# Kernel optimization log

Measured on AMD Instinct MI355X. Metric: run time of the kernel, lower is better.

## Reference

```python
import jax, jax.numpy as jnp
import numpy as np

B, N, P, Q, E = 8, 5000, 256, 256, 160000


def _linear_params(k, out_d, in_d):
    # matches nn.init.normal_(std=0.1) weights, zero bias
    return 0.1 * jax.random.normal(k, (out_d, in_d), jnp.float32), jnp.zeros((out_d,), jnp.float32)


def setup_inputs() -> dict:
    key = jax.random.key(0)
    ks = jax.random.split(key, 8)
    u = jax.random.normal(ks[0], (B, N, P + Q), jnp.float32)
    src = jax.random.randint(ks[1], (E,), 0, N, dtype=jnp.int32)
    dst = jax.random.randint(ks[2], (E,), 0, N, dtype=jnp.int32)
    t = jnp.zeros((1,), jnp.float32)
    W_Fc, b_Fc = _linear_params(ks[3], P, P + Q)
    W_Fh, b_Fh = _linear_params(ks[4], Q, P + Q)
    W_Gc, b_Gc = _linear_params(ks[5], P, P + Q)
    W_Z, b_Z = _linear_params(ks[6], P, P + Q)
    W_A, b_A = _linear_params(ks[7], Q, 2 * Q)
    return dict(u=u, src=src, dst=dst, t=t,
                W_Fc=W_Fc, b_Fc=b_Fc, W_Fh=W_Fh, b_Fh=b_Fh,
                W_Gc=W_Gc, b_Gc=b_Gc, W_Z=W_Z, b_Z=b_Z,
                W_A=W_A, b_A=b_A)


def _neighbor_mean(h, src, dst):
    # h: [B, N, Q] -> mean over in-neighbors per node (zeros if no neighbors)
    hT = jnp.transpose(h, (1, 0, 2))            # [N, B, Q]
    msgs = hT[src]                              # [E, B, Q] gather
    summed = jax.ops.segment_sum(msgs, dst, num_segments=N)          # [N, B, Q]
    deg = jax.ops.segment_sum(jnp.ones((E,), h.dtype), dst, num_segments=N)  # [N]
    mean = summed / jnp.maximum(deg, 1.0)[:, None, None]
    return jnp.transpose(mean, (1, 0, 2))       # [B, N, Q]


def reference(u, src, dst, t, W_Fc, b_Fc, W_Fh, b_Fh, W_Gc, b_Gc, W_Z, b_Z, W_A, b_A):
    sp = jax.nn.softplus
    lin = lambda x, W, b: jnp.einsum('bnd,od->bno', x, W) + b
    c = u[:, :, :P]
    h = u[:, :, P:]
    agg = _neighbor_mean(h, src, dst)                           # [B, N, Q]
    h_ = sp(lin(jnp.concatenate([h, agg], axis=2), W_A, b_A))   # [B, N, Q]
    u_ = jnp.concatenate([c, h_], axis=2)                       # [B, N, P+Q]
    Fc = sp(lin(u_, W_Fc, b_Fc))
    Gc = sp(lin(u_, W_Gc, b_Gc))
    Zt = jnp.tanh(lin(u_, W_Z, b_Z))
    Fh = sp(lin(u_, W_Fh, b_Fh))
    dc = -Fc * c + Gc * Zt
    dh = -Fh * h
    # tangent projection: remove component of dc along c
    proj = jnp.sum(dc * c, axis=2, keepdims=True) / jnp.sum(c * c, axis=2, keepdims=True)
    dc = dc - proj * c
    return jnp.concatenate([dc, dh], axis=2)
```

## Files before the change

kernel.cpp:

```cpp
#include <hip/hip_runtime.h>
#include <math.h>

#define B_ 8
#define N_ 5000
#define E_ 160000
#define M_ 40000
#define K_ 512
#define XT_ 313

typedef __bf16 v8bf __attribute__((ext_vector_type(8)));
typedef float  v4f  __attribute__((ext_vector_type(4)));
typedef unsigned short u16x4v __attribute__((ext_vector_type(4)));
typedef unsigned short u16x8v __attribute__((ext_vector_type(8)));

__device__ __forceinline__ unsigned short f2b(float f){
  unsigned int u = __builtin_bit_cast(unsigned int, f);
  u += 0x7FFFu + ((u >> 16) & 1u);
  return (unsigned short)(u >> 16);
}
__device__ __forceinline__ float b2f(unsigned short s){
  return __builtin_bit_cast(float, ((unsigned int)s) << 16);
}
__device__ __forceinline__ float softplus_(float x){
  return (x > 15.0f) ? x : __logf(1.0f + __expf(x));
}
__device__ __forceinline__ float tanh_(float x){
  float e = __expf(2.0f*x);
  return 1.0f - 2.0f/(e + 1.0f);
}


__global__ __launch_bounds__(256) void zero_int2(int* a, int* b, int n){
  int i = blockIdx.x*256 + threadIdx.x;
  if (i < n){ a[i] = 0; b[i] = 0; }
}

__global__ __launch_bounds__(256) void convert_weights(
    const float* __restrict__ wA, const float* __restrict__ wFc,
    const float* __restrict__ wGc, const float* __restrict__ wZ,
    const float* __restrict__ wFh,
    const float* __restrict__ bFc, const float* __restrict__ bGc,
    const float* __restrict__ bZ,  const float* __restrict__ bFh,
    unsigned short* __restrict__ WA, unsigned short* __restrict__ Wall,
    float* __restrict__ biasP)
{
  int idx = blockIdx.x*256 + threadIdx.x;
  if (idx >= 655360){
    int j = idx - 655360;
    int mat = j >> 8, jj = j & 255;
    const float* bp = (mat == 0) ? bFc : (mat == 1) ? bGc : (mat == 2) ? bZ : bFh;
    biasP[j] = bp[jj];
    return;
  }
  int m = idx >> 17;
  int i = idx & 131071;
  float v;
  if      (m == 0) v = wA[i];
  else if (m == 1) v = wFc[i];
  else if (m == 2) v = wGc[i];
  else if (m == 3) v = wZ[i];
  else             v = wFh[i];
  unsigned short o = f2b(v);

  int n   = (m == 0) ? (i >> 9) : ((m - 1)*256 + (i >> 9));
  int col = i & 511;
  int y  = n >> 7, nn = n & 127;
  int cb = nn >> 4, lr = nn & 15;
  int kb = col >> 6, c6 = col & 63;
  int ch = c6 >> 3, e = c6 & 7;
  int ks = ch >> 2, lq = ch & 3;
  int lane = lq*16 + lr;
  size_t pidx = ((((size_t)(y*8 + kb)*2 + ks)*8 + cb)*64 + lane)*8 + e;
  if (m == 0) WA[pidx] = o;
  else        Wall[pidx] = o;
}

__global__ __launch_bounds__(256) void convert_u(
    const float* __restrict__ u, unsigned short* __restrict__ cB,
    unsigned short* __restrict__ hT)
{
  int r = blockIdx.x*4 + (threadIdx.x >> 6);
  int l = threadIdx.x & 63;
  int n = r >> 3, b = r & 7;
  const float* up = u + (size_t)(b*N_ + n)*512 + l*4;
  float4 cf = *(const float4*)up;
  float4 hf = *(const float4*)(up + 256);
  u16x4v c4, h4;
  c4.x = f2b(cf.x); c4.y = f2b(cf.y); c4.z = f2b(cf.z); c4.w = f2b(cf.w);
  h4.x = f2b(hf.x); h4.y = f2b(hf.y); h4.z = f2b(hf.z); h4.w = f2b(hf.w);
  *(u16x4v*)(cB + (size_t)r*256 + l*4) = c4;
  *(u16x4v*)(hT + (size_t)r*256 + l*4) = h4;
}


__global__ __launch_bounds__(256) void hist_kernel(const int* __restrict__ dst, int* __restrict__ deg){
  int e = blockIdx.x*256 + threadIdx.x;
  atomicAdd(&deg[dst[e]], 1);
}

__global__ __launch_bounds__(256) void scan_kernel(
    const int* __restrict__ deg, int* __restrict__ row_start, float* __restrict__ inv_deg)
{
  __shared__ int sums[256];
  int t = threadIdx.x;
  int base = t*20;
  int cnt[20];
  int local = 0;
#pragma unroll
  for (int i = 0; i < 20; ++i){
    int n = base + i;
    int d = (n < N_) ? deg[n] : 0;
    cnt[i] = d; local += d;
  }
  sums[t] = local; __syncthreads();
  for (int s = 1; s < 256; s <<= 1){
    int v = (t >= s) ? sums[t - s] : 0;
    __syncthreads();
    sums[t] += v;
    __syncthreads();
  }
  int prefix = (t == 0) ? 0 : sums[t-1];
#pragma unroll
  for (int i = 0; i < 20; ++i){
    int n = base + i;
    if (n < N_){
      row_start[n] = prefix;
      int d = cnt[i];
      inv_deg[n] = 1.0f / (float)((d > 1) ? d : 1);
      prefix += d;
    }
  }
  if (t == 255) row_start[N_] = prefix;
}

__global__ __launch_bounds__(256) void fill_kernel(
    const int* __restrict__ src, const int* __restrict__ dst,
    const int* __restrict__ row_start, int* __restrict__ cursor, int* __restrict__ csr)
{
  int e = blockIdx.x*256 + threadIdx.x;
  int d = dst[e];
  int p = atomicAdd(&cursor[d], 1);
  csr[row_start[d] + p] = src[e];
}

__global__ __launch_bounds__(256) void gather_bn_kernel(
    const unsigned short* __restrict__ hT, const int* __restrict__ csr,
    const int* __restrict__ row_start, const float* __restrict__ inv_deg,
    unsigned short* __restrict__ aggT)
{
  const int id = blockIdx.x;
  const int bb = id & 7;
  const int g  = id >> 3;
  const int tid = threadIdx.x;
  const int n = g*4 + (tid >> 6);
  const int l = tid & 63;
  const int half = l >> 5, li = l & 31;
  const size_t coff = (size_t)bb*256 + li*8;
  const int e0 = row_start[n], e1 = row_start[n+1];

  float acc[8] = {};
  int e = e0;
  for (; e + 3 < e1; e += 4){
    const int s0 = csr[e + half];
    const int s1 = csr[e + 2 + half];
    u16x8v v0 = *(const u16x8v*)(hT + (size_t)s0*2048 + coff);
    u16x8v v1 = *(const u16x8v*)(hT + (size_t)s1*2048 + coff);
#pragma unroll
    for (int i = 0; i < 8; ++i) acc[i] += b2f(v0[i]) + b2f(v1[i]);
  }
  for (; e < e1; e += 2){
    const int idx = e + half;
    u16x8v v = {};
    if (idx < e1){
      const int s = csr[idx];
      v = *(const u16x8v*)(hT + (size_t)s*2048 + coff);
    }
#pragma unroll
    for (int i = 0; i < 8; ++i) acc[i] += b2f(v[i]);
  }
#pragma unroll
  for (int i = 0; i < 8; ++i) acc[i] += __shfl_xor(acc[i], 32, 64);

  if (half == 0){
    const float inv = inv_deg[n];
    u16x8v o;
#pragma unroll
    for (int i = 0; i < 8; ++i) o[i] = f2b(acc[i]*inv);
    *(u16x8v*)(aggT + (size_t)n*2048 + coff) = o;
  }
}


__device__ __forceinline__ void stage_a(
    const unsigned short* __restrict__ As, int m0, int ak,
    int srow, int schunk, int w, unsigned short* lbuf)
{
#pragma unroll
  for (int i = 0; i < 4; ++i){
    const unsigned short* gp = As + (size_t)(m0 + i*32 + srow)*256 + ak + schunk*8;
    unsigned short* lp = lbuf + (i*32 + w*8)*64;
    __builtin_amdgcn_global_load_lds((const __attribute__((address_space(1))) void*)gp,
                                     (__attribute__((address_space(3))) void*)lp, 16, 0, 0);
  }
}

__device__ __forceinline__ void load_b(
    const unsigned short* __restrict__ Bp, int y, int kb, int wc, int l, v8bf (&b)[8])
{
#pragma unroll
  for (int ks = 0; ks < 2; ++ks)
#pragma unroll
    for (int ct = 0; ct < 4; ++ct)
      b[ks*4+ct] = *(const v8bf*)(Bp +
          ((((size_t)(y*8 + kb)*2 + ks)*8 + wc*4 + ct)*64 + l)*8);
}

__device__ __forceinline__ void compute_tile(
    const unsigned short* lA, int wr, int lq, int lr,
    const v8bf (&bb)[8], v4f (&acc)[4][4])
{
#pragma unroll
  for (int ks = 0; ks < 2; ++ks){
    v8bf a[4];
#pragma unroll
    for (int rt = 0; rt < 4; ++rt){
      const int ar = wr*64 + rt*16 + lr;
      a[rt] = *(const v8bf*)(lA + ar*64 + (((ks*4 + lq) ^ (ar & 7)))*8);
    }
#pragma unroll
    for (int rt = 0; rt < 4; ++rt)
#pragma unroll
      for (int ct = 0; ct < 4; ++ct)
        acc[rt][ct] = __builtin_amdgcn_mfma_f32_16x16x32_bf16(a[rt], bb[ks*4+ct], acc[rt][ct], 0, 0, 0);
  }
}

template<int MODE>
__global__ __launch_bounds__(256, 3) void gemm_tiled(
    const unsigned short* __restrict__ A0, const unsigned short* __restrict__ A1,
    const unsigned short* __restrict__ Bp, const float* __restrict__ bias,
    unsigned short* dstp)
{
  const int id = blockIdx.x;
  int x, y;
  if (MODE == 1){
    const int u6 = id & 63;
    y = u6 >> 3;
    x = (id >> 6)*8 + (u6 & 7);
  } else {
    const int u4 = id & 15;
    y = u4 >> 3;
    x = (id >> 4)*8 + (u4 & 7);
  }
  if (x >= XT_) return;

  __shared__ unsigned short lds[17408];

  const int tid = threadIdx.x;
  const int w  = tid >> 6, l = tid & 63;
  const int wr = w >> 1,  wc = w & 1;
  const int lq = l >> 4,  lr = l & 15;
  const int m0 = x * 128;
  const int n0 = y * 128;

  const int srow   = tid >> 3;
  const int schunk = (tid & 7) ^ (srow & 7);

  v4f acc[4][4] = {};
  v8bf b0[8], b1[8];

  stage_a(A0, m0, 0, srow, schunk, w, lds);
  asm volatile("" ::: "memory");
  load_b(Bp, y, 0, wc, l, b0);
  asm volatile("s_waitcnt vmcnt(8)" ::: "memory");
  __builtin_amdgcn_s_barrier();
  __builtin_amdgcn_sched_barrier(0);

#pragma unroll
  for (int kb = 0; kb < 7; ++kb){
    const int kn = kb + 1;
    stage_a((kn < 4) ? A0 : A1, m0, (kn & 3)*64, srow, schunk, w,
            lds + (kn & 1)*8192);
    asm volatile("" ::: "memory");
    if (kn & 1) load_b(Bp, y, kn, wc, l, b1);
    else        load_b(Bp, y, kn, wc, l, b0);
    if (kb & 1) compute_tile(lds + 8192, wr, lq, lr, b1, acc);
    else        compute_tile(lds,        wr, lq, lr, b0, acc);
    asm volatile("s_waitcnt vmcnt(8)" ::: "memory");
    __builtin_amdgcn_s_barrier();
    __builtin_amdgcn_sched_barrier(0);
  }
  compute_tile(lds + 8192, wr, lq, lr, b1, acc);

  float bv[4];
#pragma unroll
  for (int ct = 0; ct < 4; ++ct) bv[ct] = bias[n0 + wc*64 + ct*16 + lr];

  const bool is_tanh = (MODE == 1) && ((y >> 1) == 2);

  __syncthreads();
#pragma unroll
  for (int rt = 0; rt < 4; ++rt){
#pragma unroll
    for (int ct = 0; ct < 4; ++ct){
      const int col = wc*64 + ct*16 + lr;
#pragma unroll
      for (int reg = 0; reg < 4; ++reg){
        const int row = wr*64 + rt*16 + lq*4 + reg;
        const float xv = acc[rt][ct][reg] + bv[ct];
        const float v = is_tanh ? tanh_(xv) : softplus_(xv);
        lds[row*136 + col] = f2b(v);
      }
    }
  }
  __syncthreads();

#pragma unroll
  for (int i = 0; i < 8; ++i){
    const int row = i*16 + (tid >> 4);
    const int r = m0 + row;
    if (r < M_){
      const uint4 v = *(const uint4*)(lds + row*136 + (tid & 15)*8);
      if (MODE == 0){
        *(uint4*)(dstp + (size_t)r*256 + n0 + (tid & 15)*8) = v;
      } else {
        const int n = r >> 3, b = r & 7;
        *(uint4*)(dstp + ((size_t)b*N_ + n)*1024 + n0 + (tid & 15)*8) = v;
      }
    }
  }
}


__global__ __launch_bounds__(256) void epilogue_kernel(
    const unsigned short* act, const float* __restrict__ u, float* out)
{
  int r = blockIdx.x*4 + (threadIdx.x >> 6);
  int l = threadIdx.x & 63;
  int n = r >> 3, b = r & 7;
  const size_t rr = (size_t)(b*N_ + n);
  const unsigned short* arow = act + rr*1024;
  const float* urow = u + rr*512;
  float* orow = out + rr*512;

  u16x4v fc4 = *(const u16x4v*)(arow +        l*4);
  u16x4v gc4 = *(const u16x4v*)(arow + 256 +  l*4);
  u16x4v z4  = *(const u16x4v*)(arow + 512 +  l*4);
  u16x4v fh4 = *(const u16x4v*)(arow + 768 +  l*4);
  float4 c4f = *(const float4*)(urow + l*4);
  float4 h4f = *(const float4*)(urow + 256 + l*4);

  float c[4] = {c4f.x, c4f.y, c4f.z, c4f.w};
  float h[4] = {h4f.x, h4f.y, h4f.z, h4f.w};
  float dc[4], fh[4];
  float num = 0.f, den = 0.f;
#pragma unroll
  for (int i = 0; i < 4; ++i){
    float fc = b2f(fc4[i]), gc = b2f(gc4[i]), z = b2f(z4[i]);
    fh[i] = b2f(fh4[i]);
    dc[i] = -fc*c[i] + gc*z;
    num += dc[i]*c[i];
    den += c[i]*c[i];
  }
#pragma unroll
  for (int s = 1; s < 64; s <<= 1){
    num += __shfl_xor(num, s, 64);
    den += __shfl_xor(den, s, 64);
  }
  const float proj = num / den;

  float4 o, oh;
  o.x = dc[0] - proj*c[0]; o.y = dc[1] - proj*c[1];
  o.z = dc[2] - proj*c[2]; o.w = dc[3] - proj*c[3];
  oh.x = -fh[0]*h[0]; oh.y = -fh[1]*h[1];
  oh.z = -fh[2]*h[2]; oh.w = -fh[3]*h[3];
  *(float4*)(orow + l*4) = o;
  *(float4*)(orow + 256 + l*4) = oh;
}


extern "C" void kernel_launch(void* const* d_in, const int* in_sizes, int n_in,
                              void* d_out, int out_size, void* d_ws, size_t ws_size,
                              hipStream_t stream) {
  const float* u    = (const float*)d_in[0];
  const int*   src  = (const int*)d_in[1];
  const int*   dst  = (const int*)d_in[2];
  const float* wFc  = (const float*)d_in[4];
  const float* bFc  = (const float*)d_in[5];
  const float* wFh  = (const float*)d_in[6];
  const float* bFh  = (const float*)d_in[7];
  const float* wGc  = (const float*)d_in[8];
  const float* bGc  = (const float*)d_in[9];
  const float* wZ   = (const float*)d_in[10];
  const float* bZ   = (const float*)d_in[11];
  const float* wA   = (const float*)d_in[12];
  const float* bA   = (const float*)d_in[13];
  float* out = (float*)d_out;
  unsigned short* act = (unsigned short*)d_out;

  char* W = (char*)d_ws;
  unsigned short* hT   = (unsigned short*)(W + 0);
  unsigned short* cB   = (unsigned short*)(W + 20480000);
  unsigned short* aggT = (unsigned short*)(W + 40960000);
  unsigned short* hB   = (unsigned short*)(W + 61440000);
  unsigned short* WA   = (unsigned short*)(W + 81920000);
  unsigned short* Wall = (unsigned short*)(W + 82182144);
  float* biasP   = (float*)(W + 83230720);
  int* deg       = (int*)(W + 83234816);
  int* row_start = (int*)(W + 83255296);
  int* cursor    = (int*)(W + 83275776);
  int* csr       = (int*)(W + 83296256);
  float* inv_deg = (float*)(W + 83936256);

  zero_int2<<<(N_ + 255)/256, 256, 0, stream>>>(deg, cursor, N_);
  convert_weights<<<2564, 256, 0, stream>>>(wA, wFc, wGc, wZ, wFh,
                                            bFc, bGc, bZ, bFh, WA, Wall, biasP);
  convert_u<<<M_/4, 256, 0, stream>>>(u, cB, hT);
  hist_kernel<<<E_/256, 256, 0, stream>>>(dst, deg);
  scan_kernel<<<1, 256, 0, stream>>>(deg, row_start, inv_deg);
  fill_kernel<<<E_/256, 256, 0, stream>>>(src, dst, row_start, cursor, csr);

  gather_bn_kernel<<<8*1250, 256, 0, stream>>>(hT, csr, row_start, inv_deg, aggT);

  gemm_tiled<0><<<40*16, 256, 0, stream>>>(hT, aggT, WA, bA, hB);
  gemm_tiled<1><<<40*64, 256, 0, stream>>>(cB, hB, Wall, biasP, act);

  epilogue_kernel<<<M_/4, 256, 0, stream>>>(act, u, out);
}
```

Before: 348.4 us.

## Double GEMM M-tile to 256 rows with 512-thread blocks and single B buffer

The tiled GEMM now handles 256 rows of M per block using 8 waves (512 threads), so each loaded B fragment is reused across twice as many rows and half as many blocks are launched. The B register double-buffer is replaced by a single buffer that is reloaded after each compute step, which cuts register pressure. The epilogue writes its output in two 128-row halves through LDS. In exchange, LDS per block grows to 64 KB and the B load now sits directly in front of the next compute, so its latency may be exposed.

New measurement: 439.0 us. +26.0%, slower.

```diff
diff --git a/kernel.cpp b/kernel.cpp
--- a/kernel.cpp
+++ b/kernel.cpp
@@ -6,7 +6,7 @@
 #define E_ 160000
 #define M_ 40000
 #define K_ 512
-#define XT_ 313
+#define XT2_ 157
 
 typedef __bf16 v8bf __attribute__((ext_vector_type(8)));
 typedef float  v4f  __attribute__((ext_vector_type(4)));
@@ -197,8 +197,8 @@
 {
 #pragma unroll
   for (int i = 0; i < 4; ++i){
-    const unsigned short* gp = As + (size_t)(m0 + i*32 + srow)*256 + ak + schunk*8;
-    unsigned short* lp = lbuf + (i*32 + w*8)*64;
+    const unsigned short* gp = As + (size_t)(m0 + i*64 + srow)*256 + ak + schunk*8;
+    unsigned short* lp = lbuf + (i*64 + w*8)*64;
     __builtin_amdgcn_global_load_lds((const __attribute__((address_space(1))) void*)gp,
                                      (__attribute__((address_space(3))) void*)lp, 16, 0, 0);
   }
@@ -236,7 +236,7 @@
 }
 
 template<int MODE>
-__global__ __launch_bounds__(256, 3) void gemm_tiled(
+__global__ __launch_bounds__(512, 4) void gemm_tiled(
     const unsigned short* __restrict__ A0, const unsigned short* __restrict__ A1,
     const unsigned short* __restrict__ Bp, const float* __restrict__ bias,
     unsigned short* dstp)
@@ -252,26 +252,26 @@
     y = u4 >> 3;
     x = (id >> 4)*8 + (u4 & 7);
   }
-  if (x >= XT_) return;
-
-  __shared__ unsigned short lds[17408];
+  if (x >= XT2_) return;
+
+  __shared__ unsigned short lds[32768];
 
   const int tid = threadIdx.x;
   const int w  = tid >> 6, l = tid & 63;
   const int wr = w >> 1,  wc = w & 1;
   const int lq = l >> 4,  lr = l & 15;
-  const int m0 = x * 128;
+  const int m0 = x * 256;
   const int n0 = y * 128;
 
   const int srow   = tid >> 3;
   const int schunk = (tid & 7) ^ (srow & 7);
 
   v4f acc[4][4] = {};
-  v8bf b0[8], b1[8];
+  v8bf breg[8];
 
   stage_a(A0, m0, 0, srow, schunk, w, lds);
   asm volatile("" ::: "memory");
-  load_b(Bp, y, 0, wc, l, b0);
+  load_b(Bp, y, 0, wc, l, breg);
   asm volatile("s_waitcnt vmcnt(8)" ::: "memory");
   __builtin_amdgcn_s_barrier();
   __builtin_amdgcn_sched_barrier(0);
@@ -280,17 +280,15 @@
   for (int kb = 0; kb < 7; ++kb){
     const int kn = kb + 1;
     stage_a((kn < 4) ? A0 : A1, m0, (kn & 3)*64, srow, schunk, w,
-            lds + (kn & 1)*8192);
+            lds + (kn & 1)*16384);
     asm volatile("" ::: "memory");
-    if (kn & 1) load_b(Bp, y, kn, wc, l, b1);
-    else        load_b(Bp, y, kn, wc, l, b0);
-    if (kb & 1) compute_tile(lds + 8192, wr, lq, lr, b1, acc);
-    else        compute_tile(lds,        wr, lq, lr, b0, acc);
+    compute_tile(lds + (kb & 1)*16384, wr, lq, lr, breg, acc);
+    load_b(Bp, y, kn, wc, l, breg);
     asm volatile("s_waitcnt vmcnt(8)" ::: "memory");
     __builtin_amdgcn_s_barrier();
     __builtin_amdgcn_sched_barrier(0);
   }
-  compute_tile(lds + 8192, wr, lq, lr, b1, acc);
+  compute_tile(lds + 16384, wr, lq, lr, breg, acc);
 
   float bv[4];
 #pragma unroll
@@ -300,34 +298,39 @@
 
   __syncthreads();
 #pragma unroll
-  for (int rt = 0; rt < 4; ++rt){
-#pragma unroll
-    for (int ct = 0; ct < 4; ++ct){
-      const int col = wc*64 + ct*16 + lr;
-#pragma unroll
-      for (int reg = 0; reg < 4; ++reg){
-        const int row = wr*64 + rt*16 + lq*4 + reg;
-        const float xv = acc[rt][ct][reg] + bv[ct];
-        const float v = is_tanh ? tanh_(xv) : softplus_(xv);
-        lds[row*136 + col] = f2b(v);
+  for (int h = 0; h < 2; ++h){
+    if ((wr >> 1) == h){
+#pragma unroll
+      for (int rt = 0; rt < 4; ++rt){
+#pragma unroll
+        for (int ct = 0; ct < 4; ++ct){
+          const int col = wc*64 + ct*16 + lr;
+#pragma unroll
+          for (int reg = 0; reg < 4; ++reg){
+            const int lrow = (wr & 1)*64 + rt*16 + lq*4 + reg;
+            const float xv = acc[rt][ct][reg] + bv[ct];
+            const float v = is_tanh ? tanh_(xv) : softplus_(xv);
+            lds[lrow*136 + col] = f2b(v);
+          }
+        }
       }
     }
-  }
-  __syncthreads();
-
-#pragma unroll
-  for (int i = 0; i < 8; ++i){
-    const int row = i*16 + (tid >> 4);
-    const int r = m0 + row;
-    if (r < M_){
-      const uint4 v = *(const uint4*)(lds + row*136 + (tid & 15)*8);
-      if (MODE == 0){
-        *(uint4*)(dstp + (size_t)r*256 + n0 + (tid & 15)*8) = v;
-      } else {
-        const int n = r >> 3, b = r & 7;
-        *(uint4*)(dstp + ((size_t)b*N_ + n)*1024 + n0 + (tid & 15)*8) = v;
+    __syncthreads();
+#pragma unroll
+    for (int i = 0; i < 4; ++i){
+      const int lrow = i*32 + (tid >> 4);
+      const int r = m0 + h*128 + lrow;
+      if (r < M_){
+        const uint4 v = *(const uint4*)(lds + lrow*136 + (tid & 15)*8);
+        if (MODE == 0){
+          *(uint4*)(dstp + (size_t)r*256 + n0 + (tid & 15)*8) = v;
+        } else {
+          const int n = r >> 3, b2 = r & 7;
+          *(uint4*)(dstp + ((size_t)b2*N_ + n)*1024 + n0 + (tid & 15)*8) = v;
+        }
       }
     }
+    __syncthreads();
   }
 }
 
@@ -422,8 +425,8 @@
 
   gather_bn_kernel<<<8*1250, 256, 0, stream>>>(hT, csr, row_start, inv_deg, aggT);
 
-  gemm_tiled<0><<<40*16, 256, 0, stream>>>(hT, aggT, WA, bA, hB);
-  gemm_tiled<1><<<40*64, 256, 0, stream>>>(cB, hB, Wall, biasP, act);
+  gemm_tiled<0><<<20*16, 512, 0, stream>>>(hT, aggT, WA, bA, hB);
+  gemm_tiled<1><<<20*64, 512, 0, stream>>>(cB, hB, Wall, biasP, act);
 
   epilogue_kernel<<<M_/4, 256, 0, stream>>>(act, u, out);
 }
```
